# Performance work log

Hardware: AMD Instinct MI355X
Metric: run time of the kernel (lower is better)

Reference implementation:

```python
import jax, jax.numpy as jnp
import numpy as np

EPS = 1e-12
B, S, H, NH, L, F = 8, 512, 768, 12, 12, 3072
V, TV, P = 21128, 2, 512
DH = H // NH


def layer_norm(x, g, b):
    m = jnp.mean(x, axis=-1, keepdims=True)
    v = jnp.var(x, axis=-1, keepdims=True)
    return g * (x - m) / jnp.sqrt(v + EPS) + b


def setup_inputs() -> dict:
    key = jax.random.key(0)
    ks = iter(jax.random.split(key, 40))
    r = lambda shape: (jax.random.normal(next(ks), shape, jnp.float32) * 0.02)
    inp = {
        "input_ids": jax.random.randint(next(ks), (B, S), 0, V, jnp.int32),
        "segment_ids": jax.random.randint(next(ks), (B, S), 0, TV, jnp.int32),
        "attention_mask": jnp.ones((B, 1, 1, S), jnp.float32),
        "tok_emb": r((V, H)),
        "pos_emb": r((P, H)),
        "type_emb": r((TV, H)),
        "emb_g": jnp.ones((H,), jnp.float32),
        "emb_b": jnp.zeros((H,), jnp.float32),
        # stacked per-layer params [L, ...]
        "Wq": r((L, H, H)), "bq": jnp.zeros((L, H), jnp.float32),
        "Wk": r((L, H, H)), "bk": jnp.zeros((L, H), jnp.float32),
        "Wv": r((L, H, H)), "bv": jnp.zeros((L, H), jnp.float32),
        "Wao": r((L, H, H)), "bao": jnp.zeros((L, H), jnp.float32),
        "ln1_g": jnp.ones((L, H), jnp.float32), "ln1_b": jnp.zeros((L, H), jnp.float32),
        "Wi": r((L, H, F)), "bi": jnp.zeros((L, F), jnp.float32),
        "Wio": r((L, F, H)), "bio": jnp.zeros((L, H), jnp.float32),
        "ln2_g": jnp.ones((L, H), jnp.float32), "ln2_b": jnp.zeros((L, H), jnp.float32),
    }
    return inp


def reference(input_ids, segment_ids, attention_mask,
              tok_emb, pos_emb, type_emb, emb_g, emb_b,
              Wq, bq, Wk, bk, Wv, bv, Wao, bao, ln1_g, ln1_b,
              Wi, bi, Wio, bio, ln2_g, ln2_b):
    # ---- embedding: token + type + position, then LayerNorm ----
    x = tok_emb[input_ids] + type_emb[segment_ids] + pos_emb[None, :S, :]
    x = layer_norm(x, emb_g, emb_b)  # [B,S,H]

    mask_add = (1.0 - attention_mask) * -10000.0  # [B,1,1,S]
    scale = 1.0 / jnp.sqrt(jnp.asarray(DH, x.dtype))

    def split_heads(t):  # [B,S,H] -> [B,NH,S,DH]
        return t.reshape(B, S, NH, DH).transpose(0, 2, 1, 3)

    for l in range(Wq.shape[0]):
        q = split_heads(x @ Wq[l] + bq[l])
        k = split_heads(x @ Wk[l] + bk[l])
        v = split_heads(x @ Wv[l] + bv[l])
        score = jnp.einsum("bhqd,bhkd->bhqk", q, k) * scale + mask_add
        attn = jax.nn.softmax(score, axis=-1)
        ctx = jnp.einsum("bhqk,bhkd->bhqd", attn, v)
        ctx = ctx.transpose(0, 2, 1, 3).reshape(B, S, H)
        # attention output: dense + residual + LN
        attn_out = layer_norm(ctx @ Wao[l] + bao[l] + x, ln1_g[l], ln1_b[l])
        # FFN: dense-gelu-dense + residual + LN (exact erf gelu as in tf.keras)
        h = jax.nn.gelu(attn_out @ Wi[l] + bi[l], approximate=False)
        x = layer_norm(h @ Wio[l] + bio[l] + attn_out, ln2_g[l], ln2_b[l])

    return x  # sequence output [B,S,H]
```

## Files before the change

kernel.cpp:

```cpp
#include <hip/hip_runtime.h>
#include <math.h>

static constexpr int Bc = 8;
static constexpr int Sc = 512;
static constexpr int Hc = 768;
static constexpr int NHc = 12;
static constexpr int Lc = 12;
static constexpr int Fc = 3072;
static constexpr int DHc = 64;
static constexpr int NTOK = Bc * Sc;
static constexpr int QKVN = 3 * Hc;

static constexpr size_t W_QKV_OFF = 0;
static constexpr size_t W_AO_OFF  = 1769472;
static constexpr size_t W_I_OFF   = 2359296;
static constexpr size_t W_IO_OFF  = 4718592;
static constexpr size_t LW        = 7077888;

typedef _Float16 h16x8 __attribute__((ext_vector_type(8)));
typedef float f32x4 __attribute__((ext_vector_type(4)));
typedef unsigned short us4 __attribute__((ext_vector_type(4)));
typedef unsigned short us8 __attribute__((ext_vector_type(8)));
typedef unsigned int u32x4 __attribute__((ext_vector_type(4)));

__device__ __forceinline__ unsigned short f2h(float f) {
    _Float16 h = (_Float16)f;
    return __builtin_bit_cast(unsigned short, h);
}
__device__ __forceinline__ float h2f(unsigned short u) {
    return (float)__builtin_bit_cast(_Float16, u);
}

#define AS1 __attribute__((address_space(1)))
#define AS3 __attribute__((address_space(3)))
__device__ __forceinline__ void gld_lds16(const void* g, void* l) {
    __builtin_amdgcn_global_load_lds((const AS1 void*)g, (AS3 void*)l, 16, 0, 0);
}

__global__ __launch_bounds__(256) void prep_kernel(
    const float* __restrict__ Wq, const float* __restrict__ Wk,
    const float* __restrict__ Wv, const float* __restrict__ Wao,
    const float* __restrict__ Wi, const float* __restrict__ Wio,
    const float* __restrict__ bq, const float* __restrict__ bk,
    const float* __restrict__ bv, unsigned short* __restrict__ WALL,
    float* __restrict__ BALL)
{
    int t = blockIdx.x, l = blockIdx.y;
    int tid = threadIdx.x;

    if (t >= 1728) {
        int idx = (t - 1728) * 256 + tid;
        float v = (idx < 768) ? bq[l * Hc + idx]
                : (idx < 1536) ? bk[l * Hc + idx - 768]
                               : bv[l * Hc + idx - 1536];
        BALL[(size_t)l * QKVN + idx] = v;
        return;
    }

    const float* src;
    unsigned short* dst;
    int K, N, ntn, local;
    if (t < 576) {
        int mat = t / 144; local = t % 144;
        K = 768; N = 768; ntn = 12;
        src = (mat == 0 ? Wq : mat == 1 ? Wk : mat == 2 ? Wv : Wao) + (size_t)l * 589824;
        dst = WALL + (size_t)l * LW + (mat < 3 ? (size_t)mat * 589824 : W_AO_OFF);
    } else if (t < 1152) {
        local = t - 576; K = 768; N = 3072; ntn = 48;
        src = Wi + (size_t)l * 2359296;
        dst = WALL + (size_t)l * LW + W_I_OFF;
    } else {
        local = t - 1152; K = 3072; N = 768; ntn = 12;
        src = Wio + (size_t)l * 2359296;
        dst = WALL + (size_t)l * LW + W_IO_OFF;
    }
    int n0 = (local % ntn) * 64, k0 = (local / ntn) * 64;

    __shared__ float tl[64][65];
    int tx = tid & 15, ty = tid >> 4;
#pragma unroll
    for (int j = 0; j < 4; j++) {
        int k = ty + j * 16;
        float4 v = *(const float4*)(src + (size_t)(k0 + k) * N + n0 + tx * 4);
        tl[k][tx * 4 + 0] = v.x; tl[k][tx * 4 + 1] = v.y;
        tl[k][tx * 4 + 2] = v.z; tl[k][tx * 4 + 3] = v.w;
    }
    __syncthreads();
#pragma unroll
    for (int q = 0; q < 2; q++) {
        int chunk = q * 256 + tid;
        int row = chunk >> 3, c = chunk & 7;
        us8 o;
#pragma unroll
        for (int j = 0; j < 8; j++) o[j] = f2h(tl[c * 8 + j][row]);
        *(us8*)(dst + (size_t)(n0 + row) * K + k0 + c * 8) = o;
    }
}

__device__ __forceinline__ void ln_stats192(float4 v, float& mean, float& rstd) {
    float s = v.x + v.y + v.z + v.w;
    float s2 = v.x * v.x + v.y * v.y + v.z * v.z + v.w * v.w;
#pragma unroll
    for (int o = 32; o > 0; o >>= 1) { s += __shfl_xor(s, o); s2 += __shfl_xor(s2, o); }
    __shared__ float red[6];
    int lane = threadIdx.x & 63, wid = threadIdx.x >> 6;
    if (lane == 0) { red[wid] = s; red[3 + wid] = s2; }
    __syncthreads();
    float ts  = red[0] + red[1] + red[2];
    float ts2 = red[3] + red[4] + red[5];
    mean = ts * (1.0f / Hc);
    float var = ts2 * (1.0f / Hc) - mean * mean;
    rstd = rsqrtf(var + 1e-12f);
}

__global__ __launch_bounds__(192) void embed_ln_kernel(
    const int* __restrict__ ids, const int* __restrict__ seg,
    const float* __restrict__ tok, const float* __restrict__ typ,
    const float* __restrict__ pos, const float* __restrict__ g,
    const float* __restrict__ b, float* __restrict__ outf,
    unsigned short* __restrict__ outb)
{
    int t = blockIdx.x;
    int si = t % Sc;
    int id = ids[t], sg = seg[t];
    int i = threadIdx.x;

    float4 tv = *(const float4*)(tok + (size_t)id * Hc + 4 * i);
    float4 yv = *(const float4*)(typ + (size_t)sg * Hc + 4 * i);
    float4 pv = *(const float4*)(pos + (size_t)si * Hc + 4 * i);
    float4 v = make_float4(tv.x + yv.x + pv.x, tv.y + yv.y + pv.y,
                           tv.z + yv.z + pv.z, tv.w + yv.w + pv.w);
    float mean, rstd;
    ln_stats192(v, mean, rstd);

    float4 gv = *(const float4*)(g + 4 * i);
    float4 bv = *(const float4*)(b + 4 * i);
    float4 o = make_float4(gv.x * (v.x - mean) * rstd + bv.x,
                           gv.y * (v.y - mean) * rstd + bv.y,
                           gv.z * (v.z - mean) * rstd + bv.z,
                           gv.w * (v.w - mean) * rstd + bv.w);
    *(float4*)(outf + (size_t)t * Hc + 4 * i) = o;
    us4 ob; ob[0] = f2h(o.x); ob[1] = f2h(o.y); ob[2] = f2h(o.z); ob[3] = f2h(o.w);
    *(us4*)(outb + (size_t)t * Hc + 4 * i) = ob;
}

__global__ __launch_bounds__(192) void add_ln2f_kernel(
    const float* __restrict__ t0, const float* __restrict__ t1,
    const float* __restrict__ res, const float* __restrict__ g,
    const float* __restrict__ b, float* __restrict__ outf,
    unsigned short* __restrict__ outb)
{
    int t = blockIdx.x;
    int i = threadIdx.x;
    float4 a = *(const float4*)(t0 + (size_t)t * Hc + 4 * i);
    float4 c = *(const float4*)(t1 + (size_t)t * Hc + 4 * i);
    float4 r = *(const float4*)(res + (size_t)t * Hc + 4 * i);
    float4 v = make_float4(a.x + c.x + r.x, a.y + c.y + r.y,
                           a.z + c.z + r.z, a.w + c.w + r.w);
    float mean, rstd;
    ln_stats192(v, mean, rstd);

    float4 gv = *(const float4*)(g + 4 * i);
    float4 bv = *(const float4*)(b + 4 * i);
    float4 o = make_float4(gv.x * (v.x - mean) * rstd + bv.x,
                           gv.y * (v.y - mean) * rstd + bv.y,
                           gv.z * (v.z - mean) * rstd + bv.z,
                           gv.w * (v.w - mean) * rstd + bv.w);
    *(float4*)(outf + (size_t)t * Hc + 4 * i) = o;
    us4 ob; ob[0] = f2h(o.x); ob[1] = f2h(o.y); ob[2] = f2h(o.z); ob[3] = f2h(o.w);
    *(us4*)(outb + (size_t)t * Hc + 4 * i) = ob;
}

template <int OUT>
__global__ __launch_bounds__(256) void gemm_mfma(
    const unsigned short* __restrict__ A,
    const unsigned short* __restrict__ Bt,
    const float* __restrict__ bias,
    unsigned short* __restrict__ Cb,
    unsigned short* __restrict__ VTp,
    float* __restrict__ Cf,
    int M, int N, int K, int kspan)
{
    __shared__ __align__(16) unsigned short As[128 * 64];
    __shared__ __align__(16) unsigned short Bs[128 * 64];

    int tid = threadIdx.x;
    int l = tid & 63, w = tid >> 6;
    int m0 = blockIdx.x * 128, n0 = blockIdx.y * 128;
    int lr = l & 15;
    int kg = l >> 4;
    int wr = (w >> 1) * 64, wc = (w & 1) * 64;
    int lx = lr & 7;
    int kbeg = blockIdx.z * kspan;

    f32x4 acc[4][4] = {};

    for (int k0 = kbeg; k0 < kbeg + kspan; k0 += 64) {
#pragma unroll
        for (int p = 0; p < 4; p++) {
            int i = p * 256 + w * 64 + l;
            int row = i >> 3;
            int slot = (i & 7) ^ (row & 7);
            const unsigned short* ga = A + (size_t)(m0 + row) * K + k0 + slot * 8;
            const unsigned short* gb = Bt + (size_t)(n0 + row) * K + k0 + slot * 8;
            unsigned short* la = As + (size_t)(p * 256 + w * 64) * 8;
            unsigned short* lb = Bs + (size_t)(p * 256 + w * 64) * 8;
            gld_lds16(ga, la);
            gld_lds16(gb, lb);
        }
        asm volatile("s_waitcnt vmcnt(0)" ::: "memory");
        __syncthreads();

#pragma unroll
        for (int kh = 0; kh < 2; kh++) {
            h16x8 av[4], bv[4];
#pragma unroll
            for (int f = 0; f < 4; f++) {
                int sl = (kh * 4 + kg) ^ lx;
                av[f] = *(const h16x8*)(As + (wr + f * 16 + lr) * 64 + sl * 8);
                bv[f] = *(const h16x8*)(Bs + (wc + f * 16 + lr) * 64 + sl * 8);
            }
#pragma unroll
            for (int i = 0; i < 4; i++)
#pragma unroll
                for (int j = 0; j < 4; j++)
                    acc[i][j] = __builtin_amdgcn_mfma_f32_16x16x32_f16(
                        av[i], bv[j], acc[i][j], 0, 0, 0);
        }
        __syncthreads();
    }

#pragma unroll
    for (int i = 0; i < 4; i++) {
        int rbase = m0 + wr + i * 16 + kg * 4;
#pragma unroll
        for (int j = 0; j < 4; j++) {
            int col = n0 + wc + j * 16 + lr;
            float bcol = (OUT == 4 && blockIdx.z > 0) ? 0.f : bias[col];
            if (OUT == 3 && col >= 1536) {
                int vcol = col - 1536;
                int hh = vcol >> 6, d = vcol & 63;
                int bbb = rbase >> 9, s0 = rbase & 511;
                us4 ob;
#pragma unroll
                for (int r = 0; r < 4; r++) ob[r] = f2h(acc[i][j][r] + bcol);
                *(us4*)(VTp + ((((size_t)bbb * NHc + hh) * DHc + d) << 9) + s0) = ob;
            } else if (OUT == 4) {
                float* op = Cf + (size_t)blockIdx.z * M * N;
#pragma unroll
                for (int r = 0; r < 4; r++)
                    op[(size_t)(rbase + r) * N + col] = acc[i][j][r] + bcol;
            } else {
                int ldc = (OUT == 3) ? 1536 : N;
#pragma unroll
                for (int r = 0; r < 4; r++) {
                    float v = acc[i][j][r] + bcol;
                    if (OUT == 1) v = 0.5f * v * (1.0f + erff(v * 0.70710678118654752f));
                    Cb[(size_t)(rbase + r) * ldc + col] = f2h(v);
                }
            }
        }
    }
}

__global__ __launch_bounds__(256) void attn_mfma(
    const unsigned short* __restrict__ QK, const unsigned short* __restrict__ VT,
    const float* __restrict__ mask, unsigned short* __restrict__ O)
{
    const int LD = 1536;
    __shared__ __align__(16) unsigned short Ks[64 * 64];
    __shared__ __align__(16) unsigned short Vt[64 * 64];
    __shared__ float Ml[64];

    int tid = threadIdx.x;
    int l = tid & 63, w = tid >> 6;
    int g = l >> 4, c = l & 15;
    int q0 = blockIdx.x * 64;
    int h = blockIdx.y, bb = blockIdx.z;

    const size_t rowQ = (size_t)(bb * Sc + q0 + w * 16 + c) * LD + h * DHc;
    h16x8 qv[2];
    qv[0] = *(const h16x8*)(QK + rowQ + 8 * g);
    qv[1] = *(const h16x8*)(QK + rowQ + 32 + 8 * g);

    float m_run = -1e30f, l_run = 0.f;
    f32x4 acc_o[4] = {};
    const float scale = 0.125f;

    for (int kt = 0; kt < Sc; kt += 64) {
        const unsigned short* Kgb = QK + (size_t)(bb * Sc + kt) * LD + Hc + h * DHc;
#pragma unroll
        for (int p = 0; p < 2; p++) {
            int i = p * 256 + tid;
            int row = i >> 3;
            int slot = (i & 7) ^ (row & 7);
            gld_lds16(Kgb + (size_t)row * LD + slot * 8, Ks + (size_t)(p * 256 + w * 64) * 8);
        }
        const unsigned short* Vg = VT + (((size_t)bb * NHc + h) * DHc << 9) + kt;
#pragma unroll
        for (int p = 0; p < 2; p++) {
            int i = p * 256 + tid;
            int row = i >> 3;
            int slot = (i & 7) ^ (row & 7);
            gld_lds16(Vg + ((size_t)row << 9) + slot * 8, Vt + (size_t)(p * 256 + w * 64) * 8);
        }
        if (tid < 64) Ml[tid] = (1.0f - mask[bb * Sc + kt + tid]) * -10000.0f;
        asm volatile("s_waitcnt vmcnt(0)" ::: "memory");
        __syncthreads();

        f32x4 s[4] = {};
#pragma unroll
        for (int kh = 0; kh < 2; kh++) {
#pragma unroll
            for (int f = 0; f < 4; f++) {
                int row = f * 16 + c;
                h16x8 av = *(const h16x8*)(Ks + row * 64 + (((kh * 4 + g) ^ (row & 7)) * 8));
                s[f] = __builtin_amdgcn_mfma_f32_16x16x32_f16(av, qv[kh], s[f], 0, 0, 0);
            }
        }

        f32x4 mv[4];
#pragma unroll
        for (int f = 0; f < 4; f++) mv[f] = *(const f32x4*)&Ml[f * 16 + 4 * g];
        float mx = -1e30f;
#pragma unroll
        for (int f = 0; f < 4; f++)
#pragma unroll
            for (int r = 0; r < 4; r++) {
                float sv = s[f][r] * scale + mv[f][r];
                s[f][r] = sv;
                mx = fmaxf(mx, sv);
            }
        mx = fmaxf(mx, __shfl_xor(mx, 16));
        mx = fmaxf(mx, __shfl_xor(mx, 32));
        float mn = fmaxf(m_run, mx);
        float fs = __expf(m_run - mn);
        m_run = mn;
        float ps = 0.f;
        f32x4 p[4];
#pragma unroll
        for (int f = 0; f < 4; f++)
#pragma unroll
            for (int r = 0; r < 4; r++) {
                float pv = __expf(s[f][r] - mn);
                p[f][r] = pv;
                ps += pv;
            }
        ps += __shfl_xor(ps, 16);
        ps += __shfl_xor(ps, 32);
        l_run = l_run * fs + ps;
#pragma unroll
        for (int fm = 0; fm < 4; fm++)
#pragma unroll
            for (int r = 0; r < 4; r++) acc_o[fm][r] *= fs;

        unsigned pk[4][2];
#pragma unroll
        for (int f = 0; f < 4; f++)
#pragma unroll
            for (int rp = 0; rp < 2; rp++)
                pk[f][rp] = ((unsigned)f2h(p[f][2 * rp + 1]) << 16) | f2h(p[f][2 * rp]);

#pragma unroll
        for (int kh = 0; kh < 2; kh++) {
            u32x4 bw;
#pragma unroll
            for (int t = 0; t < 4; t++) {
                int srcl = (2 * ((l >> 4) & 1) + (t >> 1)) * 16 + c;
                unsigned lo = __shfl(pk[2 * kh][t & 1], srcl);
                unsigned hi = __shfl(pk[2 * kh + 1][t & 1], srcl);
                bw[t] = (g & 2) ? hi : lo;
            }
            h16x8 bfrag = __builtin_bit_cast(h16x8, bw);
#pragma unroll
            for (int fm = 0; fm < 4; fm++) {
                int row = fm * 16 + c;
                h16x8 av = *(const h16x8*)(Vt + row * 64 + (((kh * 4 + g) ^ (row & 7)) * 8));
                acc_o[fm] = __builtin_amdgcn_mfma_f32_16x16x32_f16(av, bfrag, acc_o[fm], 0, 0, 0);
            }
        }
        __syncthreads();
    }

    float rl = 1.0f / l_run;
    size_t tokrow = (size_t)(bb * Sc + q0 + w * 16 + c) * Hc + h * DHc;
#pragma unroll
    for (int fm = 0; fm < 4; fm++) {
        us4 ob;
#pragma unroll
        for (int r = 0; r < 4; r++) ob[r] = f2h(acc_o[fm][r] * rl);
        *(us4*)(O + tokrow + fm * 16 + 4 * g) = ob;
    }
}

extern "C" void kernel_launch(void* const* d_in, const int* in_sizes, int n_in,
                              void* d_out, int out_size, void* d_ws, size_t ws_size,
                              hipStream_t stream)
{
    const int*   input_ids      = (const int*)  d_in[0];
    const int*   segment_ids    = (const int*)  d_in[1];
    const float* attention_mask = (const float*)d_in[2];
    const float* tok_emb = (const float*)d_in[3];
    const float* pos_emb = (const float*)d_in[4];
    const float* type_emb= (const float*)d_in[5];
    const float* emb_g   = (const float*)d_in[6];
    const float* emb_b   = (const float*)d_in[7];
    const float* Wq  = (const float*)d_in[8];  const float* bq  = (const float*)d_in[9];
    const float* Wk  = (const float*)d_in[10]; const float* bk  = (const float*)d_in[11];
    const float* Wv  = (const float*)d_in[12]; const float* bv  = (const float*)d_in[13];
    const float* Wao = (const float*)d_in[14]; const float* bao = (const float*)d_in[15];
    const float* ln1_g = (const float*)d_in[16]; const float* ln1_b = (const float*)d_in[17];
    const float* Wi  = (const float*)d_in[18]; const float* bi  = (const float*)d_in[19];
    const float* Wio = (const float*)d_in[20]; const float* bio = (const float*)d_in[21];
    const float* ln2_g = (const float*)d_in[22]; const float* ln2_b = (const float*)d_in[23];

    float* out = (float*)d_out;

    const size_t NT = (size_t)NTOK * Hc;
    float* Xf   = (float*)d_ws;
    float* XAf  = Xf + NT;
    float* Tf01 = XAf + NT;
    float* BALL = Tf01 + 2 * NT;
    unsigned short* QKb = (unsigned short*)(BALL + (size_t)Lc * QKVN);
    unsigned short* VT  = QKb + (size_t)NTOK * 1536;
    unsigned short* Xb  = VT + NT;
    unsigned short* XAb = Xb + NT;
    unsigned short* Cb  = XAb + NT;
    unsigned short* Hb  = Cb + NT;
    unsigned short* WALL = Hb + (size_t)NTOK * Fc;

    prep_kernel<<<dim3(1737, Lc), 256, 0, stream>>>(Wq, Wk, Wv, Wao, Wi, Wio,
                                                    bq, bk, bv, WALL, BALL);

    embed_ln_kernel<<<NTOK, 192, 0, stream>>>(input_ids, segment_ids, tok_emb,
                                              type_emb, pos_emb, emb_g, emb_b, Xf, Xb);

    dim3 gQKV(NTOK / 128, QKVN / 128);
    dim3 gF(NTOK / 128, Fc / 128);
    dim3 gH2(NTOK / 128, Hc / 128, 2);
    dim3 gA(Sc / 64, NHc, Bc);

    for (int l = 0; l < Lc; l++) {
        const unsigned short* WqkvT = WALL + (size_t)l * LW + W_QKV_OFF;
        const unsigned short* WaoT  = WALL + (size_t)l * LW + W_AO_OFF;
        const unsigned short* WiT   = WALL + (size_t)l * LW + W_I_OFF;
        const unsigned short* WioT  = WALL + (size_t)l * LW + W_IO_OFF;
        const float* bqkv = BALL + (size_t)l * QKVN;

        gemm_mfma<3><<<gQKV, 256, 0, stream>>>(Xb, WqkvT, bqkv, QKb, VT, nullptr,
                                               NTOK, QKVN, Hc, Hc);
        attn_mfma<<<gA, 256, 0, stream>>>(QKb, VT, attention_mask, Cb);

        gemm_mfma<4><<<gH2, 256, 0, stream>>>(Cb, WaoT, bao + (size_t)l * Hc, nullptr,
                                              nullptr, Tf01, NTOK, Hc, Hc, Hc / 2);
        add_ln2f_kernel<<<NTOK, 192, 0, stream>>>(Tf01, Tf01 + NT, Xf,
                                                  ln1_g + (size_t)l * Hc,
                                                  ln1_b + (size_t)l * Hc, XAf, XAb);

        gemm_mfma<1><<<gF, 256, 0, stream>>>(XAb, WiT, bi + (size_t)l * Fc, Hb, nullptr,
                                             nullptr, NTOK, Fc, Hc, Hc);
        gemm_mfma<4><<<gH2, 256, 0, stream>>>(Hb, WioT, bio + (size_t)l * Hc, nullptr,
                                              nullptr, Tf01, NTOK, Hc, Fc, Fc / 2);
        float* xout = (l == Lc - 1) ? out : Xf;
        add_ln2f_kernel<<<NTOK, 192, 0, stream>>>(Tf01, Tf01 + NT, XAf,
                                                  ln2_g + (size_t)l * Hc,
                                                  ln2_b + (size_t)l * Hc, xout, Xb);
    }
}
```

Baseline: 2.040 ms.

## Store split-K partials in fp16, remap GEMM blocks across XCDs, coarsen weight prep

The split-K GEMM partial outputs are now written as fp16 instead of fp32, and the residual-add LayerNorm kernel reads them as fp16, which halves that intermediate traffic. The GEMM maps its block ids so that neighbouring tiles land on the same XCD, to improve L2 reuse. The weight-prep kernel now processes four 64-row K slices per block, cutting its block count. Rounding the partial sums to fp16 before they are combined adds precision error.

```diff
diff --git a/kernel.cpp b/kernel.cpp
--- a/kernel.cpp
+++ b/kernel.cpp
@@ -48,8 +48,8 @@
     int t = blockIdx.x, l = blockIdx.y;
     int tid = threadIdx.x;
 
-    if (t >= 1728) {
-        int idx = (t - 1728) * 256 + tid;
+    if (t >= 432) {
+        int idx = (t - 432) * 256 + tid;
         float v = (idx < 768) ? bq[l * Hc + idx]
                 : (idx < 1536) ? bk[l * Hc + idx - 768]
                                : bv[l * Hc + idx - 1536];
@@ -59,41 +59,54 @@
 
     const float* src;
     unsigned short* dst;
-    int K, N, ntn, local;
-    if (t < 576) {
-        int mat = t / 144; local = t % 144;
-        K = 768; N = 768; ntn = 12;
+    int K, N, nkt, local;
+    if (t < 144) {
+        int mat = t / 36; local = t % 36;
+        K = 768; N = 768; nkt = 3;
         src = (mat == 0 ? Wq : mat == 1 ? Wk : mat == 2 ? Wv : Wao) + (size_t)l * 589824;
         dst = WALL + (size_t)l * LW + (mat < 3 ? (size_t)mat * 589824 : W_AO_OFF);
-    } else if (t < 1152) {
-        local = t - 576; K = 768; N = 3072; ntn = 48;
+    } else if (t < 288) {
+        local = t - 144; K = 768; N = 3072; nkt = 3;
         src = Wi + (size_t)l * 2359296;
         dst = WALL + (size_t)l * LW + W_I_OFF;
     } else {
-        local = t - 1152; K = 3072; N = 768; ntn = 12;
+        local = t - 288; K = 3072; N = 768; nkt = 12;
         src = Wio + (size_t)l * 2359296;
         dst = WALL + (size_t)l * LW + W_IO_OFF;
     }
-    int n0 = (local % ntn) * 64, k0 = (local / ntn) * 64;
+    int n0 = (local / nkt) * 64, k0 = (local % nkt) * 256;
 
     __shared__ float tl[64][65];
     int tx = tid & 15, ty = tid >> 4;
-#pragma unroll
-    for (int j = 0; j < 4; j++) {
-        int k = ty + j * 16;
-        float4 v = *(const float4*)(src + (size_t)(k0 + k) * N + n0 + tx * 4);
-        tl[k][tx * 4 + 0] = v.x; tl[k][tx * 4 + 1] = v.y;
-        tl[k][tx * 4 + 2] = v.z; tl[k][tx * 4 + 3] = v.w;
-    }
-    __syncthreads();
-#pragma unroll
-    for (int q = 0; q < 2; q++) {
-        int chunk = q * 256 + tid;
-        int row = chunk >> 3, c = chunk & 7;
-        us8 o;
-#pragma unroll
-        for (int j = 0; j < 8; j++) o[j] = f2h(tl[c * 8 + j][row]);
-        *(us8*)(dst + (size_t)(n0 + row) * K + k0 + c * 8) = o;
+    int s_own = (tid >> 3) & 3;
+    int c8    = tid & 7;
+    int rb    = tid >> 5;
+
+    us8 o[8];
+    for (int s = 0; s < 4; s++) {
+        int ks = k0 + s * 64;
+#pragma unroll
+        for (int j = 0; j < 4; j++) {
+            int k = ty + j * 16;
+            float4 v = *(const float4*)(src + (size_t)(ks + k) * N + n0 + tx * 4);
+            tl[k][tx * 4 + 0] = v.x; tl[k][tx * 4 + 1] = v.y;
+            tl[k][tx * 4 + 2] = v.z; tl[k][tx * 4 + 3] = v.w;
+        }
+        __syncthreads();
+        if (s == s_own) {
+#pragma unroll
+            for (int it = 0; it < 8; it++) {
+                int r = rb + it * 8;
+#pragma unroll
+                for (int j = 0; j < 8; j++) o[it][j] = f2h(tl[c8 * 8 + j][r]);
+            }
+        }
+        __syncthreads();
+    }
+#pragma unroll
+    for (int it = 0; it < 8; it++) {
+        int r = rb + it * 8;
+        *(us8*)(dst + (size_t)(n0 + r) * K + k0 + s_own * 64 + c8 * 8) = o[it];
     }
 }
 
@@ -144,19 +157,21 @@
     *(us4*)(outb + (size_t)t * Hc + 4 * i) = ob;
 }
 
-__global__ __launch_bounds__(192) void add_ln2f_kernel(
-    const float* __restrict__ t0, const float* __restrict__ t1,
+__global__ __launch_bounds__(192) void add_ln2h_kernel(
+    const unsigned short* __restrict__ t0, const unsigned short* __restrict__ t1,
     const float* __restrict__ res, const float* __restrict__ g,
     const float* __restrict__ b, float* __restrict__ outf,
     unsigned short* __restrict__ outb)
 {
     int t = blockIdx.x;
     int i = threadIdx.x;
-    float4 a = *(const float4*)(t0 + (size_t)t * Hc + 4 * i);
-    float4 c = *(const float4*)(t1 + (size_t)t * Hc + 4 * i);
+    us4 a = *(const us4*)(t0 + (size_t)t * Hc + 4 * i);
+    us4 c = *(const us4*)(t1 + (size_t)t * Hc + 4 * i);
     float4 r = *(const float4*)(res + (size_t)t * Hc + 4 * i);
-    float4 v = make_float4(a.x + c.x + r.x, a.y + c.y + r.y,
-                           a.z + c.z + r.z, a.w + c.w + r.w);
+    float4 v = make_float4(h2f(a[0]) + h2f(c[0]) + r.x,
+                           h2f(a[1]) + h2f(c[1]) + r.y,
+                           h2f(a[2]) + h2f(c[2]) + r.z,
+                           h2f(a[3]) + h2f(c[3]) + r.w);
     float mean, rstd;
     ln_stats192(v, mean, rstd);
 
@@ -178,7 +193,6 @@
     const float* __restrict__ bias,
     unsigned short* __restrict__ Cb,
     unsigned short* __restrict__ VTp,
-    float* __restrict__ Cf,
     int M, int N, int K, int kspan)
 {
     __shared__ __align__(16) unsigned short As[128 * 64];
@@ -186,7 +200,16 @@
 
     int tid = threadIdx.x;
     int l = tid & 63, w = tid >> 6;
-    int m0 = blockIdx.x * 128, n0 = blockIdx.y * 128;
+
+    int nbx = gridDim.x;
+    int nwg = nbx * gridDim.y;
+    int bid = blockIdx.y * nbx + blockIdx.x;
+    if ((nwg & 7) == 0) {
+        int cpx = nwg >> 3;
+        bid = (bid & 7) * cpx + (bid >> 3);
+    }
+    int m0 = (bid % nbx) * 128, n0 = (bid / nbx) * 128;
+
     int lr = l & 15;
     int kg = l >> 4;
     int wr = (w >> 1) * 64, wc = (w & 1) * 64;
@@ -246,10 +269,10 @@
                 for (int r = 0; r < 4; r++) ob[r] = f2h(acc[i][j][r] + bcol);
                 *(us4*)(VTp + ((((size_t)bbb * NHc + hh) * DHc + d) << 9) + s0) = ob;
             } else if (OUT == 4) {
-                float* op = Cf + (size_t)blockIdx.z * M * N;
+                unsigned short* op = Cb + (size_t)blockIdx.z * M * N;
 #pragma unroll
                 for (int r = 0; r < 4; r++)
-                    op[(size_t)(rbase + r) * N + col] = acc[i][j][r] + bcol;
+                    op[(size_t)(rbase + r) * N + col] = f2h(acc[i][j][r] + bcol);
             } else {
                 int ldc = (OUT == 3) ? 1536 : N;
 #pragma unroll
@@ -419,18 +442,18 @@
     const size_t NT = (size_t)NTOK * Hc;
     float* Xf   = (float*)d_ws;
     float* XAf  = Xf + NT;
-    float* Tf01 = XAf + NT;
-    float* BALL = Tf01 + 2 * NT;
+    float* BALL = XAf + NT;
     unsigned short* QKb = (unsigned short*)(BALL + (size_t)Lc * QKVN);
     unsigned short* VT  = QKb + (size_t)NTOK * 1536;
     unsigned short* Xb  = VT + NT;
     unsigned short* XAb = Xb + NT;
     unsigned short* Cb  = XAb + NT;
-    unsigned short* Hb  = Cb + NT;
+    unsigned short* Tp  = Cb + NT;
+    unsigned short* Hb  = Tp + 2 * NT;
     unsigned short* WALL = Hb + (size_t)NTOK * Fc;
 
-    prep_kernel<<<dim3(1737, Lc), 256, 0, stream>>>(Wq, Wk, Wv, Wao, Wi, Wio,
-                                                    bq, bk, bv, WALL, BALL);
+    prep_kernel<<<dim3(441, Lc), 256, 0, stream>>>(Wq, Wk, Wv, Wao, Wi, Wio,
+                                                   bq, bk, bv, WALL, BALL);
 
     embed_ln_kernel<<<NTOK, 192, 0, stream>>>(input_ids, segment_ids, tok_emb,
                                               type_emb, pos_emb, emb_g, emb_b, Xf, Xb);
@@ -447,22 +470,22 @@
         const unsigned short* WioT  = WALL + (size_t)l * LW + W_IO_OFF;
         const float* bqkv = BALL + (size_t)l * QKVN;
 
-        gemm_mfma<3><<<gQKV, 256, 0, stream>>>(Xb, WqkvT, bqkv, QKb, VT, nullptr,
+        gemm_mfma<3><<<gQKV, 256, 0, stream>>>(Xb, WqkvT, bqkv, QKb, VT,
                                                NTOK, QKVN, Hc, Hc);
         attn_mfma<<<gA, 256, 0, stream>>>(QKb, VT, attention_mask, Cb);
 
-        gemm_mfma<4><<<gH2, 256, 0, stream>>>(Cb, WaoT, bao + (size_t)l * Hc, nullptr,
-                                              nullptr, Tf01, NTOK, Hc, Hc, Hc / 2);
-        add_ln2f_kernel<<<NTOK, 192, 0, stream>>>(Tf01, Tf01 + NT, Xf,
+        gemm_mfma<4><<<gH2, 256, 0, stream>>>(Cb, WaoT, bao + (size_t)l * Hc, Tp,
+                                              nullptr, NTOK, Hc, Hc, Hc / 2);
+        add_ln2h_kernel<<<NTOK, 192, 0, stream>>>(Tp, Tp + NT, Xf,
                                                   ln1_g + (size_t)l * Hc,
                                                   ln1_b + (size_t)l * Hc, XAf, XAb);
 
-        gemm_mfma<1><<<gF, 256, 0, stream>>>(XAb, WiT, bi + (size_t)l * Fc, Hb, nullptr,
+        gemm_mfma<1><<<gF, 256, 0, stream>>>(XAb, WiT, bi + (size_t)l * Fc, Hb,
                                              nullptr, NTOK, Fc, Hc, Hc);
-        gemm_mfma<4><<<gH2, 256, 0, stream>>>(Hb, WioT, bio + (size_t)l * Hc, nullptr,
-                                              nullptr, Tf01, NTOK, Hc, Fc, Fc / 2);
+        gemm_mfma<4><<<gH2, 256, 0, stream>>>(Hb, WioT, bio + (size_t)l * Hc, Tp,
+                                              nullptr, NTOK, Hc, Fc, Fc / 2);
         float* xout = (l == Lc - 1) ? out : Xf;
-        add_ln2f_kernel<<<NTOK, 192, 0, stream>>>(Tf01, Tf01 + NT, XAf,
+        add_ln2h_kernel<<<NTOK, 192, 0, stream>>>(Tp, Tp + NT, XAf,
                                                   ln2_g + (size_t)l * Hc,
                                                   ln2_b + (size_t)l * Hc, xout, Xb);
     }
```

After: 2.041 ms. Within noise of the previous version (+0.1%).
